# Performance work log

Hardware: AMD Instinct MI355X
Metric: run time of the kernel (lower is better)

Reference implementation:

```python
import jax, jax.numpy as jnp
import numpy as np

B, BARS, BEATS, FRAC = 64, 16, 4, 8
IN_F = 10 * 47 * 2  # 940
LIN_OUT = 100
BEAT_H = 16
BAR_H = 32


def _p(key, shape, scale=0.05):
    return jax.random.normal(key, shape, dtype=jnp.float32) * scale


def setup_inputs() -> dict:
    key = jax.random.key(0)
    ks = jax.random.split(key, 16)
    return {
        "channels": jax.random.normal(ks[0], (B, BARS, BEATS, FRAC, 10, 2, 47), dtype=jnp.float32),
        "lin_w": _p(ks[1], (LIN_OUT, IN_F)),
        "lin_b": _p(ks[2], (LIN_OUT,)),
        # beats LSTM (unidirectional), PyTorch gate order i,f,g,o
        "b_wih": _p(ks[3], (4 * BEAT_H, LIN_OUT)),
        "b_whh": _p(ks[4], (4 * BEAT_H, BEAT_H)),
        "b_bih": _p(ks[5], (4 * BEAT_H,)),
        "b_bhh": _p(ks[6], (4 * BEAT_H,)),
        # bars LSTM, bidirectional: forward (f_) and reverse (r_) directions
        "f_wih": _p(ks[7], (4 * BAR_H, BEAT_H)),
        "f_whh": _p(ks[8], (4 * BAR_H, BAR_H)),
        "f_bih": _p(ks[9], (4 * BAR_H,)),
        "f_bhh": _p(ks[10], (4 * BAR_H,)),
        "r_wih": _p(ks[11], (4 * BAR_H, BEAT_H)),
        "r_whh": _p(ks[12], (4 * BAR_H, BAR_H)),
        "r_bih": _p(ks[13], (4 * BAR_H,)),
        "r_bhh": _p(ks[14], (4 * BAR_H,)),
    }


def lstm(x, wih, whh, bih, bhh):
    """PyTorch-semantics LSTM, batch_first. x: [N, T, F] -> h_seq [N, T, H]."""
    N = x.shape[0]
    H = whh.shape[1]
    # precompute input contribution for all timesteps
    xg = jnp.einsum('ntf,gf->ntg', x, wih) + (bih + bhh)  # [N, T, 4H]

    def step(carry, xt):
        h, c = carry
        gates = xt + h @ whh.T  # [N, 4H]
        i, f, g, o = jnp.split(gates, 4, axis=-1)
        c = jax.nn.sigmoid(f) * c + jax.nn.sigmoid(i) * jnp.tanh(g)
        h = jax.nn.sigmoid(o) * jnp.tanh(c)
        return (h, c), h

    h0 = jnp.zeros((N, H), x.dtype)
    _, hs = jax.lax.scan(step, (h0, h0), jnp.swapaxes(xg, 0, 1))  # [T, N, H]
    return jnp.swapaxes(hs, 0, 1)


def bilstm(x, f_wih, f_whh, f_bih, f_bhh, r_wih, r_whh, r_bih, r_bhh):
    fwd = lstm(x, f_wih, f_whh, f_bih, f_bhh)
    bwd = jnp.flip(lstm(jnp.flip(x, axis=1), r_wih, r_whh, r_bih, r_bhh), axis=1)
    return jnp.concatenate([fwd, bwd], axis=-1)


def reference(channels, lin_w, lin_b,
              b_wih, b_whh, b_bih, b_bhh,
              f_wih, f_whh, f_bih, f_bhh,
              r_wih, r_whh, r_bih, r_bhh):
    # channels: [B, bars, beats, frac, 10, 2, 47]
    x = jnp.swapaxes(channels, -1, -2)  # [..., 10, 47, 2]
    x = x.reshape(*x.shape[:4], IN_F)   # squash dims 4..6 -> 940
    x = jax.nn.relu(x @ lin_w.T + lin_b)  # [B, bars, beats, frac, 100]

    # Distributed depth=2: fold (B, bars, beats) into batch, seq over frac
    xb = x.reshape(B * BARS * BEATS, FRAC, LIN_OUT)
    beats = lstm(xb, b_wih, b_whh, b_bih, b_bhh)
    beats = beats.reshape(B, BARS, BEATS, FRAC, BEAT_H)

    # last fraction hidden state, then Distributed depth=1 over beats axis
    xl = beats[:, :, :, -1].reshape(B * BARS, BEATS, BEAT_H)
    bars = bilstm(xl, f_wih, f_whh, f_bih, f_bhh, r_wih, r_whh, r_bih, r_bhh)
    bars = bars.reshape(B, BARS, BEATS, 2 * BAR_H)
    return beats, bars
```

## Files before the change

### kernel.cpp

```cpp
#include <hip/hip_runtime.h>
#include <hip/hip_bf16.h>

typedef float f32x4 __attribute__((ext_vector_type(4)));
typedef short bf16x8 __attribute__((ext_vector_type(8)));

#define MFMA16(a, b, c) __builtin_amdgcn_mfma_f32_16x16x32_bf16(a, b, c, 0, 0, 0)

constexpr int K1  = 940;
constexpr int KP2 = 1024;
constexpr int NP  = 112;
constexpr int OSL = 136;

__device__ __forceinline__ float sigf(float x) { return 1.f / (1.f + __expf(-x)); }
__device__ __forceinline__ float tanhfast(float x) { return 2.f / (1.f + __expf(-2.f * x)) - 1.f; }

__device__ __forceinline__ short f2b(float x) {
  __hip_bfloat16 b = __float2bfloat16(x);
  return *reinterpret_cast<short*>(&b);
}

__global__ void prep_kernel(const float* __restrict__ lin_w,
                            const float* __restrict__ b_wih,
                            __hip_bfloat16* __restrict__ w2,
                            __hip_bfloat16* __restrict__ bw2) {
  int idx = blockIdx.x * 256 + threadIdx.x;
  if (idx < NP * KP2) {
    int n = idx >> 10, k = idx & 1023;
    float v = 0.f;
    if (n < 100 && k < K1) {
      int c10 = k / 94, rem = k - c10 * 94;
      int c2 = rem / 47, c47 = rem - c2 * 47;
      int f = c10 * 94 + c47 * 2 + c2;
      v = lin_w[n * K1 + f];
    }
    w2[idx] = __float2bfloat16(v);
  } else {
    int i2 = idx - NP * KP2;
    if (i2 < 64 * 128) {
      int g = i2 >> 7, k = i2 & 127;
      bw2[i2] = __float2bfloat16((k < 100) ? b_wih[g * 100 + k] : 0.f);
    }
  }
}

__global__ __launch_bounds__(512, 2)
void fused_encoder(const float* __restrict__ ch,
                   const __hip_bfloat16* __restrict__ w2,
                   const float* __restrict__ lin_b,
                   const __hip_bfloat16* __restrict__ bw2,
                   const float* __restrict__ bih,
                   const float* __restrict__ bhh,
                   const float* __restrict__ whh,
                   float* __restrict__ beats) {
  __shared__ float red[8 * 16 * NP];
  __shared__ __align__(16) __hip_bfloat16 out_s[64 * OSL];
  __shared__ float xg_s[64 * 65];
  const int tid = threadIdx.x;
  const int w = tid >> 6, lane = tid & 63;
  const int l16 = lane & 15, bq = lane >> 4;
  const int kbase = w * 128;

  bf16x8 breg[4][7];
#pragma unroll
  for (int s = 0; s < 4; ++s)
#pragma unroll
    for (int nt = 0; nt < 7; ++nt)
      breg[s][nt] = *reinterpret_cast<const bf16x8*>(
          &w2[(nt * 16 + l16) * KP2 + kbase + s * 32 + bq * 8]);

  const int mbase = blockIdx.x * 64;

  auto issueA = [&](int m0, float4* buf) {
    const float* ar = ch + (long)(m0 + l16) * K1 + kbase + bq * 8;
    if (w < 7) {
#pragma unroll
      for (int s = 0; s < 4; ++s) {
        buf[2 * s]     = *reinterpret_cast<const float4*>(ar + s * 32);
        buf[2 * s + 1] = *reinterpret_cast<const float4*>(ar + s * 32 + 4);
      }
    } else {
      buf[0] = *reinterpret_cast<const float4*>(ar);
      buf[1] = *reinterpret_cast<const float4*>(ar + 4);
      float t[8];
#pragma unroll
      for (int j = 0; j < 8; ++j) {
        int k = 928 + bq * 8 + j;
        t[j] = (k < K1) ? ar[32 + j] : 0.f;
      }
      buf[2] = float4{t[0], t[1], t[2], t[3]};
      buf[3] = float4{t[4], t[5], t[6], t[7]};
      buf[4] = buf[5] = buf[6] = buf[7] = float4{0.f, 0.f, 0.f, 0.f};
    }
  };

  float4 a0[8], a1[8];
  issueA(mbase, a0);

#pragma unroll
  for (int i = 0; i < 4; ++i) {
    float4* cur = (i & 1) ? a1 : a0;
    float4* nxt = (i & 1) ? a0 : a1;
    if (i < 3) issueA(mbase + (i + 1) * 16, nxt);

    f32x4 acc[7] = {};
#pragma unroll
    for (int s = 0; s < 4; ++s) {
      float4 lo = cur[2 * s], hi = cur[2 * s + 1];
      bf16x8 a = bf16x8{f2b(lo.x), f2b(lo.y), f2b(lo.z), f2b(lo.w),
                        f2b(hi.x), f2b(hi.y), f2b(hi.z), f2b(hi.w)};
#pragma unroll
      for (int nt = 0; nt < 7; ++nt) acc[nt] = MFMA16(a, breg[s][nt], acc[nt]);
    }

#pragma unroll
    for (int nt = 0; nt < 7; ++nt)
#pragma unroll
      for (int r = 0; r < 4; ++r)
        red[(w * 16 + bq * 4 + r) * NP + nt * 16 + l16] = acc[nt][r];
    __syncthreads();

    if (tid < 448) {
      const int col = tid % NP;
      const int rb = (tid / NP) * 4;
      const float bias = (col < 100) ? lin_b[col] : 0.f;
#pragma unroll
      for (int r = 0; r < 4; ++r) {
        float s = 0.f;
#pragma unroll
        for (int ww = 0; ww < 8; ++ww) s += red[(ww * 16 + rb + r) * NP + col];
        float v = fmaxf(s + bias, 0.f);
        out_s[(i * 16 + rb + r) * OSL + col] = __float2bfloat16((col < 100) ? v : 0.f);
      }
    } else {
      const int t2 = tid - 448;
      const int row = t2 >> 2, c0 = 112 + (t2 & 3) * 4;
#pragma unroll
      for (int q = 0; q < 4; ++q)
        out_s[(i * 16 + row) * OSL + c0 + q] = __float2bfloat16(0.f);
    }
    __syncthreads();
  }

  {
    const int rt = w >> 1, gt0 = (w & 1) * 2;
    bf16x8 av[4];
#pragma unroll
    for (int s = 0; s < 4; ++s)
      av[s] = *reinterpret_cast<const bf16x8*>(&out_s[(rt * 16 + l16) * OSL + s * 32 + bq * 8]);
    f32x4 xacc[2] = {{0.f, 0.f, 0.f, 0.f}, {0.f, 0.f, 0.f, 0.f}};
#pragma unroll
    for (int g2 = 0; g2 < 2; ++g2) {
      const int gt = gt0 + g2;
#pragma unroll
      for (int s = 0; s < 4; ++s) {
        bf16x8 b = *reinterpret_cast<const bf16x8*>(&bw2[(gt * 16 + l16) * 128 + s * 32 + bq * 8]);
        xacc[g2] = MFMA16(av[s], b, xacc[g2]);
      }
    }
#pragma unroll
    for (int g2 = 0; g2 < 2; ++g2) {
      const int gate = (gt0 + g2) * 16 + l16;
      const float bias = bih[gate] + bhh[gate];
#pragma unroll
      for (int r = 0; r < 4; ++r)
        xg_s[(rt * 16 + bq * 4 + r) * 65 + gate] = xacc[g2][r] + bias;
    }
  }
  __syncthreads();

  {
    const int cell = lane & 15;
    float wr[16];
#pragma unroll
    for (int u = 0; u < 16; ++u) wr[u] = whh[lane * 16 + u];
    float xv[8];
#pragma unroll
    for (int t = 0; t < 8; ++t) xv[t] = xg_s[(w * 8 + t) * 65 + lane];
    float h[16];
#pragma unroll
    for (int u = 0; u < 16; ++u) h[u] = 0.f;
    float c = 0.f;
    const int seq = blockIdx.x * 8 + w;
#pragma unroll
    for (int t = 0; t < 8; ++t) {
      float pre = xv[t];
#pragma unroll
      for (int u = 0; u < 16; ++u) pre += wr[u] * h[u];
      float act = (lane >= 32 && lane < 48) ? tanhfast(pre) : sigf(pre);
      float gi = __shfl(act, cell);
      float gf = __shfl(act, cell + 16);
      float gg = __shfl(act, cell + 32);
      float go = __shfl(act, cell + 48);
      c = gf * c + gi * gg;
      float hn = go * tanhfast(c);
#pragma unroll
      for (int u = 0; u < 16; ++u) h[u] = __shfl(hn, u);
      if (lane < 16) beats[seq * 128 + t * 16 + lane] = hn;
    }
  }
}

__global__ __launch_bounds__(256)
void bars_bilstm(const float* __restrict__ fwih, const float* __restrict__ fwhh,
                 const float* __restrict__ fbih, const float* __restrict__ fbhh,
                 const float* __restrict__ rwih, const float* __restrict__ rwhh,
                 const float* __restrict__ rbih, const float* __restrict__ rbhh,
                 const float* __restrict__ beats,
                 float* __restrict__ bars) {
  const int tid = threadIdx.x;
  const int dir = tid >> 7, g = tid & 127;
  const int n = blockIdx.x;
  const float* wih = dir ? rwih : fwih;
  const float* whh = dir ? rwhh : fwhh;
  const float bias = dir ? (rbih[g] + rbhh[g]) : (fbih[g] + fbhh[g]);
  float wi[16], wh[32];
#pragma unroll
  for (int u = 0; u < 16; ++u) wi[u] = wih[g * 16 + u];
#pragma unroll
  for (int u = 0; u < 32; ++u) wh[u] = whh[g * 32 + u];
  __shared__ float xbuf[2][16];
  __shared__ float hbuf[2][32];
  __shared__ float gact[2][128];
  float c = 0.f;
  if (g < 32) hbuf[dir][g] = 0.f;
  __syncthreads();
  for (int t = 0; t < 4; ++t) {
    const int tt = dir ? (3 - t) : t;
    if (g < 16) xbuf[dir][g] = beats[((n * 4 + tt) * 8 + 7) * 16 + g];
    __syncthreads();
    float pre = bias;
#pragma unroll
    for (int u = 0; u < 16; ++u) pre += wi[u] * xbuf[dir][u];
#pragma unroll
    for (int u = 0; u < 32; ++u) pre += wh[u] * hbuf[dir][u];
    gact[dir][g] = (g >= 64 && g < 96) ? tanhfast(pre) : sigf(pre);
    __syncthreads();
    if (g < 32) {
      c = gact[dir][32 + g] * c + gact[dir][g] * gact[dir][64 + g];
      float hn = gact[dir][96 + g] * tanhfast(c);
      hbuf[dir][g] = hn;
      bars[(n * 4 + tt) * 64 + dir * 32 + g] = hn;
    }
    __syncthreads();
  }
}

extern "C" void kernel_launch(void* const* d_in, const int* in_sizes, int n_in,
                              void* d_out, int out_size, void* d_ws, size_t ws_size,
                              hipStream_t stream) {
  const float* ch    = (const float*)d_in[0];
  const float* lin_w = (const float*)d_in[1];
  const float* lin_b = (const float*)d_in[2];
  const float* b_wih = (const float*)d_in[3];
  const float* b_whh = (const float*)d_in[4];
  const float* b_bih = (const float*)d_in[5];
  const float* b_bhh = (const float*)d_in[6];
  const float* f_wih = (const float*)d_in[7];
  const float* f_whh = (const float*)d_in[8];
  const float* f_bih = (const float*)d_in[9];
  const float* f_bhh = (const float*)d_in[10];
  const float* r_wih = (const float*)d_in[11];
  const float* r_whh = (const float*)d_in[12];
  const float* r_bih = (const float*)d_in[13];
  const float* r_bhh = (const float*)d_in[14];

  char* ws = (char*)d_ws;
  __hip_bfloat16* w2  = (__hip_bfloat16*)ws;
  __hip_bfloat16* bw2 = (__hip_bfloat16*)(ws + 229376);
  float*          out = (float*)d_out;

  prep_kernel<<<480, 256, 0, stream>>>(lin_w, b_wih, w2, bw2);
  fused_encoder<<<512, 512, 0, stream>>>(ch, w2, lin_b, bw2, b_bih, b_bhh,
                                         b_whh, out);
  bars_bilstm<<<1024, 256, 0, stream>>>(f_wih, f_whh, f_bih, f_bhh,
                                        r_wih, r_whh, r_bih, r_bhh,
                                        out, out + 524288);
}
```

Measured before the change: 240.3 us.

## Replace split-K register GEMM with LDS double-buffered M/N-tiled GEMM

The linear-layer GEMM previously split K across the 8 waves, held weights in registers and reduced partial sums through a large shared buffer. It now streams 128-wide K chunks of activations and pre-padded weight tiles into double-buffered LDS, and each wave computes its own 16x64 output tile without a cross-wave reduction. The prep kernel lays the weights out chunk-major with a padded row stride to match. This drops the reduction traffic and its extra barriers, but adds two barriers per K chunk and reloads weights from global memory in every block.

```diff
diff --git a/kernel.cpp b/kernel.cpp
--- a/kernel.cpp
+++ b/kernel.cpp
@@ -7,9 +7,8 @@
 #define MFMA16(a, b, c) __builtin_amdgcn_mfma_f32_16x16x32_bf16(a, b, c, 0, 0, 0)
 
 constexpr int K1  = 940;
-constexpr int KP2 = 1024;
-constexpr int NP  = 112;
-constexpr int OSL = 136;
+constexpr int LDR = 136;
+constexpr int BCH = 128 * LDR;
 
 __device__ __forceinline__ float sigf(float x) { return 1.f / (1.f + __expf(-x)); }
 __device__ __forceinline__ float tanhfast(float x) { return 2.f / (1.f + __expf(-2.f * x)) - 1.f; }
@@ -21,21 +20,23 @@
 
 __global__ void prep_kernel(const float* __restrict__ lin_w,
                             const float* __restrict__ b_wih,
-                            __hip_bfloat16* __restrict__ w2,
+                            __hip_bfloat16* __restrict__ w2cp,
                             __hip_bfloat16* __restrict__ bw2) {
   int idx = blockIdx.x * 256 + threadIdx.x;
-  if (idx < NP * KP2) {
-    int n = idx >> 10, k = idx & 1023;
+  if (idx < 8 * BCH) {
+    int c = idx / BCH, r = idx - c * BCH;
+    int n = r / LDR, kp = r - n * LDR;
+    int k = c * 128 + kp;
     float v = 0.f;
-    if (n < 100 && k < K1) {
+    if (n < 100 && kp < 128 && k < K1) {
       int c10 = k / 94, rem = k - c10 * 94;
       int c2 = rem / 47, c47 = rem - c2 * 47;
       int f = c10 * 94 + c47 * 2 + c2;
       v = lin_w[n * K1 + f];
     }
-    w2[idx] = __float2bfloat16(v);
+    w2cp[idx] = __float2bfloat16(v);
   } else {
-    int i2 = idx - NP * KP2;
+    int i2 = idx - 8 * BCH;
     if (i2 < 64 * 128) {
       int g = i2 >> 7, k = i2 & 127;
       bw2[i2] = __float2bfloat16((k < 100) ? b_wih[g * 100 + k] : 0.f);
@@ -45,115 +46,109 @@
 
 __global__ __launch_bounds__(512, 2)
 void fused_encoder(const float* __restrict__ ch,
-                   const __hip_bfloat16* __restrict__ w2,
+                   const __hip_bfloat16* __restrict__ w2cp,
                    const float* __restrict__ lin_b,
                    const __hip_bfloat16* __restrict__ bw2,
                    const float* __restrict__ bih,
                    const float* __restrict__ bhh,
                    const float* __restrict__ whh,
                    float* __restrict__ beats) {
-  __shared__ float red[8 * 16 * NP];
-  __shared__ __align__(16) __hip_bfloat16 out_s[64 * OSL];
+  __shared__ __align__(16) __hip_bfloat16 As[2][64 * LDR];
+  __shared__ __align__(16) __hip_bfloat16 Bs[2][128 * LDR];
+  __shared__ __align__(16) __hip_bfloat16 out_s[64 * LDR];
   __shared__ float xg_s[64 * 65];
   const int tid = threadIdx.x;
   const int w = tid >> 6, lane = tid & 63;
   const int l16 = lane & 15, bq = lane >> 4;
-  const int kbase = w * 128;
-
-  bf16x8 breg[4][7];
-#pragma unroll
-  for (int s = 0; s < 4; ++s)
-#pragma unroll
-    for (int nt = 0; nt < 7; ++nt)
-      breg[s][nt] = *reinterpret_cast<const bf16x8*>(
-          &w2[(nt * 16 + l16) * KP2 + kbase + s * 32 + bq * 8]);
-
   const int mbase = blockIdx.x * 64;
-
-  auto issueA = [&](int m0, float4* buf) {
-    const float* ar = ch + (long)(m0 + l16) * K1 + kbase + bq * 8;
-    if (w < 7) {
-#pragma unroll
-      for (int s = 0; s < 4; ++s) {
-        buf[2 * s]     = *reinterpret_cast<const float4*>(ar + s * 32);
-        buf[2 * s + 1] = *reinterpret_cast<const float4*>(ar + s * 32 + 4);
+  const int msub = (w >> 1) * 16;
+  const int nb = (w & 1) * 64;
+
+  float4 sa[4];
+  uint4 sb[5];
+
+  auto issue = [&](int c) {
+    const int kb = c * 128;
+#pragma unroll
+    for (int p = 0; p < 4; ++p) {
+      int idx = p * 512 + tid;
+      int row = idx >> 5, c4 = idx & 31;
+      int col = kb + c4 * 4;
+      sa[p] = (col < K1)
+                  ? *reinterpret_cast<const float4*>(ch + (long)(mbase + row) * K1 + col)
+                  : float4{0.f, 0.f, 0.f, 0.f};
+    }
+    const __hip_bfloat16* src = w2cp + c * BCH;
+#pragma unroll
+    for (int p = 0; p < 5; ++p) {
+      int idx = p * 512 + tid;
+      if (idx < 2176) sb[p] = *reinterpret_cast<const uint4*>(src + idx * 8);
+    }
+  };
+
+  auto stage = [&](int buf) {
+#pragma unroll
+    for (int p = 0; p < 4; ++p) {
+      int idx = p * 512 + tid;
+      int row = idx >> 5, c4 = idx & 31;
+      short4 v = {f2b(sa[p].x), f2b(sa[p].y), f2b(sa[p].z), f2b(sa[p].w)};
+      *reinterpret_cast<short4*>(&As[buf][row * LDR + c4 * 4]) = v;
+    }
+#pragma unroll
+    for (int p = 0; p < 5; ++p) {
+      int idx = p * 512 + tid;
+      if (idx < 2176) *reinterpret_cast<uint4*>(&Bs[buf][idx * 8]) = sb[p];
+    }
+  };
+
+  f32x4 acc[4] = {};
+  issue(0);
+  for (int c = 0; c < 8; ++c) {
+    const int buf = c & 1;
+    __syncthreads();
+    stage(buf);
+    __syncthreads();
+    if (c < 7) issue(c + 1);
+#pragma unroll
+    for (int s = 0; s < 4; ++s) {
+      bf16x8 a = *reinterpret_cast<const bf16x8*>(
+          &As[buf][(msub + l16) * LDR + s * 32 + bq * 8]);
+#pragma unroll
+      for (int nt = 0; nt < 4; ++nt) {
+        bf16x8 b = *reinterpret_cast<const bf16x8*>(
+            &Bs[buf][(nb + nt * 16 + l16) * LDR + s * 32 + bq * 8]);
+        acc[nt] = MFMA16(a, b, acc[nt]);
       }
-    } else {
-      buf[0] = *reinterpret_cast<const float4*>(ar);
-      buf[1] = *reinterpret_cast<const float4*>(ar + 4);
-      float t[8];
-#pragma unroll
-      for (int j = 0; j < 8; ++j) {
-        int k = 928 + bq * 8 + j;
-        t[j] = (k < K1) ? ar[32 + j] : 0.f;
-      }
-      buf[2] = float4{t[0], t[1], t[2], t[3]};
-      buf[3] = float4{t[4], t[5], t[6], t[7]};
-      buf[4] = buf[5] = buf[6] = buf[7] = float4{0.f, 0.f, 0.f, 0.f};
-    }
-  };
-
-  float4 a0[8], a1[8];
-  issueA(mbase, a0);
-
-#pragma unroll
-  for (int i = 0; i < 4; ++i) {
-    float4* cur = (i & 1) ? a1 : a0;
-    float4* nxt = (i & 1) ? a0 : a1;
-    if (i < 3) issueA(mbase + (i + 1) * 16, nxt);
-
-    f32x4 acc[7] = {};
-#pragma unroll
-    for (int s = 0; s < 4; ++s) {
-      float4 lo = cur[2 * s], hi = cur[2 * s + 1];
-      bf16x8 a = bf16x8{f2b(lo.x), f2b(lo.y), f2b(lo.z), f2b(lo.w),
-                        f2b(hi.x), f2b(hi.y), f2b(hi.z), f2b(hi.w)};
-#pragma unroll
-      for (int nt = 0; nt < 7; ++nt) acc[nt] = MFMA16(a, breg[s][nt], acc[nt]);
-    }
-
-#pragma unroll
-    for (int nt = 0; nt < 7; ++nt)
-#pragma unroll
-      for (int r = 0; r < 4; ++r)
-        red[(w * 16 + bq * 4 + r) * NP + nt * 16 + l16] = acc[nt][r];
-    __syncthreads();
-
-    if (tid < 448) {
-      const int col = tid % NP;
-      const int rb = (tid / NP) * 4;
-      const float bias = (col < 100) ? lin_b[col] : 0.f;
-#pragma unroll
-      for (int r = 0; r < 4; ++r) {
-        float s = 0.f;
-#pragma unroll
-        for (int ww = 0; ww < 8; ++ww) s += red[(ww * 16 + rb + r) * NP + col];
-        float v = fmaxf(s + bias, 0.f);
-        out_s[(i * 16 + rb + r) * OSL + col] = __float2bfloat16((col < 100) ? v : 0.f);
-      }
-    } else {
-      const int t2 = tid - 448;
-      const int row = t2 >> 2, c0 = 112 + (t2 & 3) * 4;
-#pragma unroll
-      for (int q = 0; q < 4; ++q)
-        out_s[(i * 16 + row) * OSL + c0 + q] = __float2bfloat16(0.f);
-    }
-    __syncthreads();
-  }
+    }
+  }
+
+#pragma unroll
+  for (int nt = 0; nt < 4; ++nt) {
+    const int n = nb + nt * 16 + l16;
+    const float bias = (n < 100) ? lin_b[n] : 0.f;
+#pragma unroll
+    for (int r = 0; r < 4; ++r) {
+      float v = fmaxf(acc[nt][r] + bias, 0.f);
+      out_s[(msub + bq * 4 + r) * LDR + n] = __float2bfloat16(v);
+    }
+  }
+  __syncthreads();
 
   {
     const int rt = w >> 1, gt0 = (w & 1) * 2;
     bf16x8 av[4];
 #pragma unroll
     for (int s = 0; s < 4; ++s)
-      av[s] = *reinterpret_cast<const bf16x8*>(&out_s[(rt * 16 + l16) * OSL + s * 32 + bq * 8]);
+      av[s] = *reinterpret_cast<const bf16x8*>(
+          &out_s[(rt * 16 + l16) * LDR + s * 32 + bq * 8]);
     f32x4 xacc[2] = {{0.f, 0.f, 0.f, 0.f}, {0.f, 0.f, 0.f, 0.f}};
 #pragma unroll
     for (int g2 = 0; g2 < 2; ++g2) {
       const int gt = gt0 + g2;
 #pragma unroll
       for (int s = 0; s < 4; ++s) {
-        bf16x8 b = *reinterpret_cast<const bf16x8*>(&bw2[(gt * 16 + l16) * 128 + s * 32 + bq * 8]);
+        bf16x8 b = *reinterpret_cast<const bf16x8*>(
+            &bw2[(gt * 16 + l16) * 128 + s * 32 + bq * 8]);
         xacc[g2] = MFMA16(av[s], b, xacc[g2]);
       }
     }
@@ -265,12 +260,12 @@
   const float* r_bhh = (const float*)d_in[14];
 
   char* ws = (char*)d_ws;
-  __hip_bfloat16* w2  = (__hip_bfloat16*)ws;
-  __hip_bfloat16* bw2 = (__hip_bfloat16*)(ws + 229376);
-  float*          out = (float*)d_out;
-
-  prep_kernel<<<480, 256, 0, stream>>>(lin_w, b_wih, w2, bw2);
-  fused_encoder<<<512, 512, 0, stream>>>(ch, w2, lin_b, bw2, b_bih, b_bhh,
+  __hip_bfloat16* w2cp = (__hip_bfloat16*)ws;
+  __hip_bfloat16* bw2  = (__hip_bfloat16*)(ws + 278528);
+  float*          out  = (float*)d_out;
+
+  prep_kernel<<<576, 256, 0, stream>>>(lin_w, b_wih, w2cp, bw2);
+  fused_encoder<<<512, 512, 0, stream>>>(ch, w2cp, lin_b, bw2, b_bih, b_bhh,
                                          b_whh, out);
   bars_bilstm<<<1024, 256, 0, stream>>>(f_wih, f_whh, f_bih, f_bhh,
                                         r_wih, r_whh, r_bih, r_bhh,
```

After: 266.9 us. 1.11x slower.
